# Optimization experiments

Hardware: AMD Instinct MI355X
Metric: run time of the kernel (lower is better)

Reference implementation:

```python
import jax, jax.numpy as jnp
import numpy as np

B, S, HID = 2, 2048, 2048
H, HKV, D = 16, 4, 128

def _rope(x, cos, sin):
    # x: [B,h,S,D]; cos/sin: [1,1,S,D//2]
    d = x.shape[-1] // 2
    x1, x2 = x[..., :d], x[..., d:]
    y1 = x1 * cos + x2 * sin
    y2 = -x1 * sin + x2 * cos
    return jnp.concatenate([y1, y2], axis=-1)

def _rmsnorm(x):
    eps = jnp.finfo(x.dtype).eps
    return x * jax.lax.rsqrt(jnp.mean(jnp.square(x), axis=-1, keepdims=True) + eps)

def setup_inputs() -> dict:
    key = jax.random.key(0)
    ks = jax.random.split(key, 5)
    x = jax.random.normal(ks[0], (B, S, HID), dtype=jnp.float32)
    # realistic rotary tables
    half = D // 2
    inv_freq = 1.0 / (10000.0 ** (jnp.arange(half, dtype=jnp.float32) / half))
    t = jnp.arange(S, dtype=jnp.float32)
    freqs = t[:, None] * inv_freq[None, :]            # [S, D//2]
    cos = jnp.cos(freqs)[None, None]                  # [1,1,S,D//2]
    sin = jnp.sin(freqs)[None, None]
    s = 0.02
    Wq = jax.random.normal(ks[1], (H * D, HID), dtype=jnp.float32) * s
    Wk = jax.random.normal(ks[2], (HKV * D, HID), dtype=jnp.float32) * s
    Wv = jax.random.normal(ks[3], (HKV * D, HID), dtype=jnp.float32) * s
    Wo = jax.random.normal(ks[4], (HID, H * D), dtype=jnp.float32) * s
    return {"x": x, "cos": cos, "sin": sin, "Wq": Wq, "Wk": Wk, "Wv": Wv, "Wo": Wo}

def reference(x, cos, sin, Wq, Wk, Wv, Wo):
    b, s, _ = x.shape
    rep = H // HKV
    q = (x @ Wq.T).reshape(b, s, H, D).transpose(0, 2, 1, 3)      # [B,H,S,D]
    k = (x @ Wk.T).reshape(b, s, HKV, D).transpose(0, 2, 1, 3)    # [B,Hkv,S,D]
    v = (x @ Wv.T).reshape(b, s, HKV, D).transpose(0, 2, 1, 3)
    k = jnp.repeat(k, rep, axis=1)                                # GQA expand
    v = jnp.repeat(v, rep, axis=1)
    q = _rmsnorm(_rope(q, cos, sin))
    k = _rmsnorm(_rope(k, cos, sin))
    scores = jnp.einsum('bhqd,bhkd->bhqk', q, k) * (D ** -0.5)
    causal = jnp.tril(jnp.ones((s, s), dtype=bool))
    scores = jnp.where(causal, scores, -jnp.inf)
    attn = jax.nn.softmax(scores, axis=-1)
    out = jnp.einsum('bhqk,bhkd->bhqd', attn, v)                  # [B,H,S,D]
    out = out.transpose(0, 2, 1, 3).reshape(b, s, H * D)
    return out @ Wo.T
```

## Files before the change

### kernel.cpp

```cpp
#include <hip/hip_runtime.h>
#include <hip/hip_bf16.h>

#define B_  2
#define S_  2048
#define HID_ 2048
#define H_  16
#define HKV_ 4
#define D_  128

typedef __bf16 bf16_t;
typedef bf16_t bf16x8 __attribute__((ext_vector_type(8)));
typedef float f32x4 __attribute__((ext_vector_type(4)));

typedef __attribute__((address_space(3))) unsigned int lds_u32_t;
typedef const __attribute__((address_space(1))) unsigned int glob_u32_t;

__device__ __forceinline__ void gl2lds16(const bf16_t* g, bf16_t* l) {
    __builtin_amdgcn_global_load_lds((glob_u32_t*)g, (lds_u32_t*)l, 16, 0, 0);
}

__device__ __forceinline__ unsigned packbf2(float a, float b) {
    union { bf16_t h[2]; unsigned u; } p;
    p.h[0] = (bf16_t)a;
    p.h[1] = (bf16_t)b;
    return p.u;
}

__global__ void detect_dtype(const unsigned* __restrict__ x, int* __restrict__ flag) {
    int lane = threadIdx.x;
    int c = 0;
#pragma unroll
    for (int i = 0; i < 16; ++i) {
        unsigned w = x[lane * 16 + i];
        unsigned e = (w >> 7) & 0xFF;
        c += (e >= 117 && e <= 137) ? 1 : 0;
    }
#pragma unroll
    for (int m = 1; m < 64; m <<= 1) c += __shfl_xor(c, m, 64);
    if (lane == 0) *flag = (c >= 512) ? 1 : 0;
}

struct Cseg { const void* src; bf16_t* dst; int n8; };

__global__ __launch_bounds__(256) void convert_bf16(Cseg s0, Cseg s1, Cseg s2, Cseg s3,
                                                    const int* __restrict__ flagp) {
    Cseg s = (blockIdx.y == 0) ? s0 : (blockIdx.y == 1) ? s1 : (blockIdx.y == 2) ? s2 : s3;
    const int i = blockIdx.x * 256 + threadIdx.x;
    if (i >= s.n8) return;
    if (*flagp) {
        ((uint4*)s.dst)[i] = ((const uint4*)s.src)[i];
    } else {
        const float4* p = (const float4*)s.src + (size_t)i * 2;
        float4 u = p[0], v = p[1];
        bf16x8 r;
        r[0] = (bf16_t)u.x; r[1] = (bf16_t)u.y; r[2] = (bf16_t)u.z; r[3] = (bf16_t)u.w;
        r[4] = (bf16_t)v.x; r[5] = (bf16_t)v.y; r[6] = (bf16_t)v.z; r[7] = (bf16_t)v.w;
        *(bf16x8*)(s.dst + (size_t)i * 8) = r;
    }
}

__global__ __launch_bounds__(256) void gemm_lds(const bf16_t* __restrict__ A,
                                                const bf16_t* __restrict__ W,
                                                void* __restrict__ C,
                                                int M, int N, int K,
                                                const int* __restrict__ flagp, int osel) {
    __shared__ bf16_t As[128 * 32];
    __shared__ bf16_t Bs[128 * 32];

    const int tid = threadIdx.x;
    const int w = tid >> 6;
    const int lane = tid & 63;
    const int r = lane & 15;
    const int quad = lane >> 4;
    const int m0 = blockIdx.y * 128;
    const int n0 = blockIdx.x * 128;
    const bool of32 = osel && (*flagp == 0);

    const int mh = (w & 1) * 64;
    const int nh = (w >> 1) * 64;

    const int c0 = w * 2;
    const int srow = lane >> 2;
    const int scol = (lane & 3) * 8;
    const bf16_t* Ag0 = A + (size_t)(m0 + c0 * 16 + srow) * K + scol;
    const bf16_t* Ag1 = A + (size_t)(m0 + c0 * 16 + 16 + srow) * K + scol;
    const bf16_t* Wg0 = W + (size_t)(n0 + c0 * 16 + srow) * K + scol;
    const bf16_t* Wg1 = W + (size_t)(n0 + c0 * 16 + 16 + srow) * K + scol;
    bf16_t* Al0 = As + c0 * 512;
    bf16_t* Al1 = As + (c0 + 1) * 512;
    bf16_t* Bl0 = Bs + c0 * 512;
    bf16_t* Bl1 = Bs + (c0 + 1) * 512;

    f32x4 acc[4][4] = {};

    for (int k0 = 0; k0 < K; k0 += 32) {
        __syncthreads();
        gl2lds16(Ag0 + k0, Al0);
        gl2lds16(Ag1 + k0, Al1);
        gl2lds16(Wg0 + k0, Bl0);
        gl2lds16(Wg1 + k0, Bl1);
        __syncthreads();

        bf16x8 a[4], b[4];
#pragma unroll
        for (int mi = 0; mi < 4; ++mi)
            a[mi] = *(const bf16x8*)&As[(mh + mi * 16 + r) * 32 + quad * 8];
#pragma unroll
        for (int ni = 0; ni < 4; ++ni)
            b[ni] = *(const bf16x8*)&Bs[(nh + ni * 16 + r) * 32 + quad * 8];
#pragma unroll
        for (int mi = 0; mi < 4; ++mi)
#pragma unroll
            for (int ni = 0; ni < 4; ++ni)
                acc[mi][ni] = __builtin_amdgcn_mfma_f32_16x16x32_bf16(a[mi], b[ni], acc[mi][ni], 0, 0, 0);
    }

#pragma unroll
    for (int mi = 0; mi < 4; ++mi) {
#pragma unroll
        for (int ni = 0; ni < 4; ++ni) {
#pragma unroll
            for (int g = 0; g < 4; ++g) {
                const int row = m0 + mh + mi * 16 + quad * 4 + g;
                const int col = n0 + nh + ni * 16 + r;
                if (of32) ((float*)C)[(size_t)row * N + col] = acc[mi][ni][g];
                else ((__hip_bfloat16*)C)[(size_t)row * N + col] = __float2bfloat16(acc[mi][ni][g]);
            }
        }
    }
}

template <bool F32>
__device__ __forceinline__ bf16x8 load8(const void* base, size_t off) {
    bf16x8 r;
    if constexpr (F32) {
        const float4* p = (const float4*)((const float*)base + off);
        float4 u = p[0], v = p[1];
        r[0] = (bf16_t)u.x; r[1] = (bf16_t)u.y; r[2] = (bf16_t)u.z; r[3] = (bf16_t)u.w;
        r[4] = (bf16_t)v.x; r[5] = (bf16_t)v.y; r[6] = (bf16_t)v.z; r[7] = (bf16_t)v.w;
    } else {
        r = *(const bf16x8*)((const bf16_t*)base + off);
    }
    return r;
}

template <bool AF32, bool WF32, bool OF32>
__device__ __forceinline__ void gemm_body(const void* __restrict__ A, const void* __restrict__ W,
                                          void* __restrict__ C, int M, int N, int K) {
    const int wave = threadIdx.x >> 6;
    const int lane = threadIdx.x & 63;
    const int r = lane & 15;
    const int quad = lane >> 4;
    const int m0 = blockIdx.y * 64 + wave * 16;
    const int n0 = blockIdx.x * 64;

    f32x4 acc[4] = {};
    const size_t aoff = (size_t)(m0 + r) * K + quad * 8;
    const size_t woff = (size_t)(n0 + r) * K + quad * 8;

    for (int k0 = 0; k0 < K; k0 += 32) {
        bf16x8 a = load8<AF32>(A, aoff + k0);
#pragma unroll
        for (int ns = 0; ns < 4; ++ns) {
            bf16x8 b = load8<WF32>(W, woff + (size_t)(ns * 16) * K + k0);
            acc[ns] = __builtin_amdgcn_mfma_f32_16x16x32_bf16(a, b, acc[ns], 0, 0, 0);
        }
    }

#pragma unroll
    for (int ns = 0; ns < 4; ++ns) {
#pragma unroll
        for (int reg = 0; reg < 4; ++reg) {
            int m = m0 + quad * 4 + reg;
            int n = n0 + ns * 16 + r;
            if constexpr (OF32) ((float*)C)[(size_t)m * N + n] = acc[ns][reg];
            else ((__hip_bfloat16*)C)[(size_t)m * N + n] = __float2bfloat16(acc[ns][reg]);
        }
    }
}

__global__ __launch_bounds__(256) void gemm_bt(const void* __restrict__ A, const void* __restrict__ W,
                                               void* __restrict__ C, int M, int N, int K,
                                               const int* __restrict__ flagp, int mode) {
    const int bf = *flagp;
    if (bf) {
        gemm_body<false, false, false>(A, W, C, M, N, K);
    } else if (mode == 0) {
        gemm_body<true, true, false>(A, W, C, M, N, K);
    } else {
        gemm_body<false, true, true>(A, W, C, M, N, K);
    }
}

__global__ __launch_bounds__(256) void rope_rms(__hip_bfloat16* __restrict__ qk,
                                                const void* __restrict__ cosp,
                                                const void* __restrict__ sinp,
                                                int NH, int ld, const int* __restrict__ flagp) {
    const int bf = *flagp;
    const int wave = threadIdx.x >> 6;
    const int lane = threadIdx.x & 63;
    const int row = blockIdx.x * 4 + wave;
    const int h = row % NH;
    const int bs = row / NH;
    const int s = bs % S_;

    __hip_bfloat16* p = qk + (size_t)bs * ld + h * D_;
    float x1 = __bfloat162float(p[lane]);
    float x2 = __bfloat162float(p[lane + 64]);
    float c, sn, eps;
    if (bf) {
        c   = __bfloat162float(((const __hip_bfloat16*)cosp)[s * 64 + lane]);
        sn  = __bfloat162float(((const __hip_bfloat16*)sinp)[s * 64 + lane]);
        eps = 0.0078125f;
    } else {
        c   = ((const float*)cosp)[s * 64 + lane];
        sn  = ((const float*)sinp)[s * 64 + lane];
        eps = 1.1920929e-07f;
    }
    float y1 = x1 * c + x2 * sn;
    float y2 = x2 * c - x1 * sn;
    float ss = y1 * y1 + y2 * y2;
#pragma unroll
    for (int m = 1; m < 64; m <<= 1) ss += __shfl_xor(ss, m, 64);
    float rinv = rsqrtf(ss * (1.0f / 128.0f) + eps);
    p[lane]      = __float2bfloat16(y1 * rinv);
    p[lane + 64] = __float2bfloat16(y2 * rinv);
}

__global__ __launch_bounds__(256) void v_pack(const __hip_bfloat16* __restrict__ V,
                                              unsigned* __restrict__ Vp, int ldv) {
    const int idx = blockIdx.x * 256 + threadIdx.x;
    const int kp = idx & 15;
    const int t  = (idx >> 4) & 63;
    const int d  = (idx >> 10) & 127;
    const int gy = idx >> 17;
    const int kvh = gy & 3;
    const int b = gy >> 2;
    const unsigned short* p = (const unsigned short*)V
        + (size_t)(b * S_ + 32 * t + kp) * ldv + kvh * D_ + d;
    unsigned lo = p[0];
    unsigned hi = p[(size_t)16 * ldv];
    Vp[idx] = lo | (hi << 16);
}

__global__ __launch_bounds__(512, 2) void attn_flash4(const __hip_bfloat16* __restrict__ Q,
                                                      const __hip_bfloat16* __restrict__ K,
                                                      const unsigned* __restrict__ Vp,
                                                      __hip_bfloat16* __restrict__ O,
                                                      int ldq, int ldkv, int ldo) {
    __shared__ unsigned Pb[8][2][16][16];
    __shared__ float Of[4][32][128];
    __shared__ float Ml[4][2][2][16];

    const int tid = threadIdx.x;
    const int w = tid >> 6;
    const int lane = tid & 63;
    const int r = lane & 15;
    const int quad = lane >> 4;

    const int id = blockIdx.x;
    const int gy = id & 7;
    const int px = id >> 3;
    const int kvh = gy & 3;
    const int b = gy >> 2;
    const int hh = w & 3;
    const int half = w >> 2;
    const int h = kvh * 4 + hh;

    const bf16_t* Kg = (const bf16_t*)K + (size_t)b * S_ * ldkv + kvh * D_;
    const unsigned* Vg = Vp + (size_t)gy * (D_ * 64 * 16);

    bf16x8 ones;
#pragma unroll
    for (int j = 0; j < 8; ++j) ones[j] = (bf16_t)1.0f;

    const float SC2 = 0.08838834764831845f * 1.4426950408889634f;

    for (int rep = 0; rep < 2; ++rep) {
        const int qt = rep ? (63 - px) : px;
        const int q0 = qt * 32;
        const int nkt = qt + 1;
        const int ktb = half ? (nkt >> 1) : 0;
        const int kte = half ? nkt : (nkt >> 1);

        bf16x8 qf[2][4];
#pragma unroll
        for (int t = 0; t < 2; ++t) {
            const bf16_t* qp = (const bf16_t*)Q + (size_t)(b * S_ + q0 + t * 16 + r) * ldq + h * D_ + quad * 8;
#pragma unroll
            for (int c = 0; c < 4; ++c) qf[t][c] = *(const bf16x8*)(qp + c * 32);
        }

        f32x4 oacc[2][8] = {};
        f32x4 lacc[2] = {};
        float m_i[2][4];
#pragma unroll
        for (int t = 0; t < 2; ++t)
#pragma unroll
            for (int g = 0; g < 4; ++g) m_i[t][g] = -3e38f;

        for (int kt = ktb; kt < kte; ++kt) {
            const int k0 = kt * 32;
            const bf16_t* kp0 = Kg + (size_t)(k0 + r) * ldkv + quad * 8;

            f32x4 s0[2] = {}, s1[2] = {};
            __builtin_amdgcn_s_setprio(1);
#pragma unroll
            for (int c = 0; c < 4; ++c) {
                bf16x8 kb0 = *(const bf16x8*)(kp0 + c * 32);
                bf16x8 kb1 = *(const bf16x8*)(kp0 + (size_t)16 * ldkv + c * 32);
#pragma unroll
                for (int t = 0; t < 2; ++t) {
                    s0[t] = __builtin_amdgcn_mfma_f32_16x16x32_bf16(qf[t][c], kb0, s0[t], 0, 0, 0);
                    s1[t] = __builtin_amdgcn_mfma_f32_16x16x32_bf16(qf[t][c], kb1, s1[t], 0, 0, 0);
                }
            }
            __builtin_amdgcn_s_setprio(0);

            const bool bnd = (kt == qt);
#pragma unroll
            for (int t = 0; t < 2; ++t) {
                float mt[4];
#pragma unroll
                for (int g = 0; g < 4; ++g) {
                    s0[t][g] *= SC2;
                    s1[t][g] *= SC2;
                    if (bnd) {
                        const int qrow = q0 + t * 16 + quad * 4 + g;
                        if (k0 + r > qrow)      s0[t][g] = -1e38f;
                        if (k0 + 16 + r > qrow) s1[t][g] = -1e38f;
                    }
                    mt[g] = fmaxf(s0[t][g], s1[t][g]);
                }
#pragma unroll
                for (int msk = 1; msk < 16; msk <<= 1) {
#pragma unroll
                    for (int g = 0; g < 4; ++g) mt[g] = fmaxf(mt[g], __shfl_xor(mt[g], msk, 64));
                }
                bool upd = false;
#pragma unroll
                for (int g = 0; g < 4; ++g) upd |= (mt[g] > m_i[t][g]);
                if (__ballot(upd)) {
#pragma unroll
                    for (int g = 0; g < 4; ++g) {
                        const float mn = fmaxf(m_i[t][g], mt[g]);
                        const float al = exp2f(m_i[t][g] - mn);
                        m_i[t][g] = mn;
                        lacc[t][g] *= al;
#pragma unroll
                        for (int ns = 0; ns < 8; ++ns) oacc[t][ns][g] *= al;
                    }
                }
#pragma unroll
                for (int g = 0; g < 4; ++g) {
                    const float p0 = exp2f(s0[t][g] - m_i[t][g]);
                    const float p1 = exp2f(s1[t][g] - m_i[t][g]);
                    const int row = quad * 4 + g;
                    Pb[w][t][row][(((r >> 2) ^ quad) & 3) * 4 + (r & 3)] = packbf2(p0, p1);
                }
            }

            const int pgrp = ((quad ^ (r >> 2)) & 3) * 4;
            bf16x8 pf0 = *(const bf16x8*)&Pb[w][0][r][pgrp];
            bf16x8 pf1 = *(const bf16x8*)&Pb[w][1][r][pgrp];

            lacc[0] = __builtin_amdgcn_mfma_f32_16x16x32_bf16(pf0, ones, lacc[0], 0, 0, 0);
            lacc[1] = __builtin_amdgcn_mfma_f32_16x16x32_bf16(pf1, ones, lacc[1], 0, 0, 0);

            const unsigned* vp = Vg + (size_t)r * (64 * 16) + kt * 16 + quad * 4;
            __builtin_amdgcn_s_setprio(1);
#pragma unroll
            for (int ns = 0; ns < 8; ++ns) {
                bf16x8 vf = *(const bf16x8*)(vp + (size_t)ns * 16 * 64 * 16);
                oacc[0][ns] = __builtin_amdgcn_mfma_f32_16x16x32_bf16(pf0, vf, oacc[0][ns], 0, 0, 0);
                oacc[1][ns] = __builtin_amdgcn_mfma_f32_16x16x32_bf16(pf1, vf, oacc[1][ns], 0, 0, 0);
            }
            __builtin_amdgcn_s_setprio(0);
        }

        if (half) {
#pragma unroll
            for (int t = 0; t < 2; ++t) {
                if (r == 0) {
#pragma unroll
                    for (int g = 0; g < 4; ++g) {
                        Ml[hh][t][0][quad * 4 + g] = m_i[t][g];
                        Ml[hh][t][1][quad * 4 + g] = lacc[t][g];
                    }
                }
#pragma unroll
                for (int ns = 0; ns < 8; ++ns)
#pragma unroll
                    for (int g = 0; g < 4; ++g)
                        Of[hh][t * 16 + quad * 4 + g][ns * 16 + r] = oacc[t][ns][g];
            }
        }
        __syncthreads();
        if (!half) {
#pragma unroll
            for (int t = 0; t < 2; ++t) {
#pragma unroll
                for (int g = 0; g < 4; ++g) {
                    const int r16 = quad * 4 + g;
                    const float mB = Ml[hh][t][0][r16];
                    const float lB = Ml[hh][t][1][r16];
                    const float mA = m_i[t][g];
                    const float mx = fmaxf(mA, mB);
                    const float aA = exp2f(mA - mx);
                    const float aB = exp2f(mB - mx);
                    const float inv = 1.0f / (lacc[t][g] * aA + lB * aB);
                    const int qrow = q0 + t * 16 + r16;
                    __hip_bfloat16* op = O + (size_t)(b * S_ + qrow) * ldo + h * D_;
#pragma unroll
                    for (int ns = 0; ns < 8; ++ns) {
                        const float v = (oacc[t][ns][g] * aA + Of[hh][t * 16 + r16][ns * 16 + r] * aB) * inv;
                        op[ns * 16 + r] = __float2bfloat16(v);
                    }
                }
            }
        }
        __syncthreads();
    }
}

#define KT_ 32
#define LDK 136

__global__ __launch_bounds__(256, 2) void attn_flash3(const __hip_bfloat16* __restrict__ Q,
                                                      const __hip_bfloat16* __restrict__ K,
                                                      const __hip_bfloat16* __restrict__ V,
                                                      __hip_bfloat16* __restrict__ O,
                                                      int ldq, int ldkv, int ldo) {
    __shared__ unsigned short Ks[KT_][LDK];
    __shared__ unsigned int Vt[D_ * 16];
    __shared__ unsigned int Pb[4][2][16][16];

    const int tid = threadIdx.x;
    const int w = tid >> 6;
    const int lane = tid & 63;
    const int r = lane & 15;
    const int quad = lane >> 4;

    const int gy = blockIdx.y;
    const int kvh = gy % HKV_;
    const int b = gy / HKV_;
    const int qt = b ? blockIdx.x : (gridDim.x - 1 - blockIdx.x);
    const int q0 = qt * 32;
    const int h = kvh * 4 + w;

    bf16x8 qf[2][4];
#pragma unroll
    for (int t = 0; t < 2; ++t) {
        const bf16_t* qp = (const bf16_t*)Q + (size_t)(b * S_ + q0 + t * 16 + r) * ldq + h * D_ + quad * 8;
#pragma unroll
        for (int c = 0; c < 4; ++c) qf[t][c] = *(const bf16x8*)(qp + c * 32);
    }

    f32x4 oacc[2][8] = {};
    f32x4 lacc[2] = {};
    float m_i[2][4];
#pragma unroll
    for (int t = 0; t < 2; ++t)
#pragma unroll
        for (int g = 0; g < 4; ++g) m_i[t][g] = -3e38f;

    const bf16_t* Kg = (const bf16_t*)K + (size_t)b * S_ * ldkv + kvh * D_;
    const bf16_t* Vg = (const bf16_t*)V + (size_t)b * S_ * ldkv + kvh * D_;

    bf16x8 ones;
#pragma unroll
    for (int j = 0; j < 8; ++j) ones[j] = (bf16_t)1.0f;

    const float SC2 = 0.08838834764831845f * 1.4426950408889634f;

    const int skey = tid >> 4;
    const int sdc = tid & 15;
    union U4 { uint4 u; unsigned short s[8]; };
    U4 rk0, rk1, rv0, rv1;
    {
        const size_t o0 = (size_t)skey * ldkv + sdc * 8;
        const size_t o1 = o0 + (size_t)16 * ldkv;
        rk0.u = *(const uint4*)(Kg + o0);
        rk1.u = *(const uint4*)(Kg + o1);
        rv0.u = *(const uint4*)(Vg + o0);
        rv1.u = *(const uint4*)(Vg + o1);
    }

    for (int kt = 0; kt <= qt; ++kt) {
        const int k0 = kt * KT_;
        __syncthreads();
        *(uint4*)&Ks[skey][sdc * 8] = rk0.u;
        *(uint4*)&Ks[skey + 16][sdc * 8] = rk1.u;
#pragma unroll
        for (int j = 0; j < 8; ++j) {
            const int d = sdc * 8 + j;
            const int f = ((j >> 1) & 3) ^ (sdc & 3);
            const int grp = (skey >> 2) ^ f;
            Vt[d * 16 + grp * 4 + (skey & 3)] = (unsigned)rv0.s[j] | ((unsigned)rv1.s[j] << 16);
        }
        __syncthreads();
        if (kt < qt) {
            const size_t o0 = (size_t)(k0 + KT_ + skey) * ldkv + sdc * 8;
            const size_t o1 = o0 + (size_t)16 * ldkv;
            rk0.u = *(const uint4*)(Kg + o0);
            rk1.u = *(const uint4*)(Kg + o1);
            rv0.u = *(const uint4*)(Vg + o0);
            rv1.u = *(const uint4*)(Vg + o1);
        }

        f32x4 s0[2] = {}, s1[2] = {};
#pragma unroll
        for (int c = 0; c < 4; ++c) {
            bf16x8 kb0 = *(const bf16x8*)&Ks[r][c * 32 + quad * 8];
            bf16x8 kb1 = *(const bf16x8*)&Ks[16 + r][c * 32 + quad * 8];
#pragma unroll
            for (int t = 0; t < 2; ++t) {
                s0[t] = __builtin_amdgcn_mfma_f32_16x16x32_bf16(qf[t][c], kb0, s0[t], 0, 0, 0);
                s1[t] = __builtin_amdgcn_mfma_f32_16x16x32_bf16(qf[t][c], kb1, s1[t], 0, 0, 0);
            }
        }

        const bool bnd = (kt == qt);
#pragma unroll
        for (int t = 0; t < 2; ++t) {
            float mt[4];
#pragma unroll
            for (int g = 0; g < 4; ++g) {
                s0[t][g] *= SC2;
                s1[t][g] *= SC2;
                if (bnd) {
                    const int qrow = q0 + t * 16 + quad * 4 + g;
                    if (k0 + r > qrow)      s0[t][g] = -1e38f;
                    if (k0 + 16 + r > qrow) s1[t][g] = -1e38f;
                }
                mt[g] = fmaxf(s0[t][g], s1[t][g]);
            }
#pragma unroll
            for (int msk = 1; msk < 16; msk <<= 1) {
#pragma unroll
                for (int g = 0; g < 4; ++g) mt[g] = fmaxf(mt[g], __shfl_xor(mt[g], msk, 64));
            }
            bool upd = false;
#pragma unroll
            for (int g = 0; g < 4; ++g) upd |= (mt[g] > m_i[t][g]);
            if (__ballot(upd)) {
#pragma unroll
                for (int g = 0; g < 4; ++g) {
                    const float mn = fmaxf(m_i[t][g], mt[g]);
                    const float al = exp2f(m_i[t][g] - mn);
                    m_i[t][g] = mn;
                    lacc[t][g] *= al;
#pragma unroll
                    for (int ns = 0; ns < 8; ++ns) oacc[t][ns][g] *= al;
                }
            }
#pragma unroll
            for (int g = 0; g < 4; ++g) {
                const float p0 = exp2f(s0[t][g] - m_i[t][g]);
                const float p1 = exp2f(s1[t][g] - m_i[t][g]);
                const int row = quad * 4 + g;
                Pb[w][t][row][(((r >> 2) ^ quad) & 3) * 4 + (r & 3)] = packbf2(p0, p1);
            }
        }

        const int pgrp = ((quad ^ (r >> 2)) & 3) * 4;
        bf16x8 pf0 = *(const bf16x8*)&Pb[w][0][r][pgrp];
        bf16x8 pf1 = *(const bf16x8*)&Pb[w][1][r][pgrp];

        lacc[0] = __builtin_amdgcn_mfma_f32_16x16x32_bf16(pf0, ones, lacc[0], 0, 0, 0);
        lacc[1] = __builtin_amdgcn_mfma_f32_16x16x32_bf16(pf1, ones, lacc[1], 0, 0, 0);

#pragma unroll
        for (int ns = 0; ns < 8; ++ns) {
            const int d = ns * 16 + r;
            const int f = ((r >> 1) & 3) ^ ((2 * ns + (r >> 3)) & 3);
            bf16x8 vf = *(const bf16x8*)&Vt[d * 16 + ((quad ^ f) & 3) * 4];
            oacc[0][ns] = __builtin_amdgcn_mfma_f32_16x16x32_bf16(pf0, vf, oacc[0][ns], 0, 0, 0);
            oacc[1][ns] = __builtin_amdgcn_mfma_f32_16x16x32_bf16(pf1, vf, oacc[1][ns], 0, 0, 0);
        }
    }

#pragma unroll
    for (int t = 0; t < 2; ++t) {
#pragma unroll
        for (int g = 0; g < 4; ++g) {
            const float inv = 1.0f / lacc[t][g];
            const int qrow = q0 + t * 16 + quad * 4 + g;
            __hip_bfloat16* op = O + (size_t)(b * S_ + qrow) * ldo + h * D_;
#pragma unroll
            for (int ns = 0; ns < 8; ++ns)
                op[ns * 16 + r] = __float2bfloat16(oacc[t][ns][g] * inv);
        }
    }
}

extern "C" void kernel_launch(void* const* d_in, const int* in_sizes, int n_in,
                              void* d_out, int out_size, void* d_ws, size_t ws_size,
                              hipStream_t stream) {
    const void* x    = d_in[0];
    const void* cosp = d_in[1];
    const void* sinp = d_in[2];
    const void* Wq   = d_in[3];
    const void* Wk   = d_in[4];
    const void* Wv   = d_in[5];
    const void* Wo   = d_in[6];

    const int M = B_ * S_;
    const size_t MB = 1ull << 20;

    if (ws_size >= 28 * MB + 64) {
        char* ws = (char*)d_ws;
        bf16_t* xb = (bf16_t*)ws;
        bf16_t* wb = (bf16_t*)(ws + 16 * MB);
        bf16_t* wo = (bf16_t*)(ws + 16 * MB);
        unsigned* vp4 = (unsigned*)(ws + 24 * MB);
        bf16_t* ao = (bf16_t*)ws;
        int* flag  = (int*)(ws + 28 * MB);
        bf16_t* qkv = (bf16_t*)d_out;

        detect_dtype<<<1, 64, 0, stream>>>((const unsigned*)x, flag);

        Cseg sx{x,  xb,                          (B_ * S_ * HID_) / 8};
        Cseg sq{Wq, wb,                          (H_ * D_ * HID_) / 8};
        Cseg sk{Wk, wb + (size_t)2048 * HID_,    (HKV_ * D_ * HID_) / 8};
        Cseg sv{Wv, wb + (size_t)2560 * HID_,    (HKV_ * D_ * HID_) / 8};
        convert_bf16<<<dim3(4096, 4), 256, 0, stream>>>(sx, sq, sk, sv, flag);

        gemm_lds<<<dim3(3072 / 128, M / 128), 256, 0, stream>>>(xb, wb, qkv, M, 3072, HID_, flag, 0);

        Cseg so{Wo, wo, (HID_ * H_ * D_) / 8};
        convert_bf16<<<dim3(2048, 1), 256, 0, stream>>>(so, so, so, so, flag);

        v_pack<<<(B_ * HKV_ * D_ * 64 * 16) / 256, 256, 0, stream>>>(
            (const __hip_bfloat16*)(qkv + 2560), vp4, 3072);

        rope_rms<<<(B_ * S_ * H_) / 4, 256, 0, stream>>>((__hip_bfloat16*)qkv, cosp, sinp, H_, 3072, flag);
        rope_rms<<<(B_ * S_ * HKV_) / 4, 256, 0, stream>>>((__hip_bfloat16*)(qkv + 2048), cosp, sinp, HKV_, 3072, flag);

        attn_flash4<<<dim3(256), 512, 0, stream>>>(
            (const __hip_bfloat16*)qkv, (const __hip_bfloat16*)(qkv + 2048),
            vp4, (__hip_bfloat16*)ao, 3072, 3072, 2048);

        gemm_lds<<<dim3(HID_ / 128, M / 128), 256, 0, stream>>>(ao, wo, d_out, M, HID_, H_ * D_, flag, 1);
    } else {
        __hip_bfloat16* qb = (__hip_bfloat16*)d_ws;
        int* flag = (int*)((char*)d_ws + (size_t)M * (H_ * D_) * sizeof(__hip_bfloat16));
        __hip_bfloat16* kb = (__hip_bfloat16*)d_out;
        __hip_bfloat16* vb = kb + (size_t)M * (HKV_ * D_);

        detect_dtype<<<1, 64, 0, stream>>>((const unsigned*)x, flag);

        gemm_bt<<<dim3((H_ * D_) / 64, M / 64), 256, 0, stream>>>(x, Wq, qb, M, H_ * D_, HID_, flag, 0);
        gemm_bt<<<dim3((HKV_ * D_) / 64, M / 64), 256, 0, stream>>>(x, Wk, kb, M, HKV_ * D_, HID_, flag, 0);
        gemm_bt<<<dim3((HKV_ * D_) / 64, M / 64), 256, 0, stream>>>(x, Wv, vb, M, HKV_ * D_, HID_, flag, 0);

        rope_rms<<<(B_ * S_ * H_) / 4, 256, 0, stream>>>(qb, cosp, sinp, H_, H_ * D_, flag);
        rope_rms<<<(B_ * S_ * HKV_) / 4, 256, 0, stream>>>(kb, cosp, sinp, HKV_, HKV_ * D_, flag);

        attn_flash3<<<dim3(S_ / 32, B_ * HKV_), 256, 0, stream>>>(qb, kb, vb, qb, H_ * D_, HKV_ * D_, H_ * D_);

        gemm_bt<<<dim3(HID_ / 64, M / 64), 256, 0, stream>>>(qb, Wo, d_out, M, HID_, H_ * D_, flag, 1);
    }
}
```

Measured before the change: 416.9 us.

## Drop online softmax max using fixed offset, split KV four ways, pack K/V tile-contiguous

Because q and k are RMS-normalized, scores are bounded, so the kernel replaces the running max and rescaling with a constant exponent offset and removes the shuffle reductions and ballot-driven rescales. The attention block grows to 1024 threads with the KV range split across four wave groups, merged sequentially through LDS. A new k_pack kernel and a reordered v_pack lay out K and V contiguously per 32-key tile for better locality. This relies on the norm bound (the fixed offset could overflow or underflow for other inputs), adds extra syncthreads in the merge, and adds a pack pass plus a stricter requirement on the output buffer size.

```diff
diff --git a/kernel.cpp b/kernel.cpp
--- a/kernel.cpp
+++ b/kernel.cpp
@@ -227,30 +227,44 @@
     p[lane + 64] = __float2bfloat16(y2 * rinv);
 }
 
+__global__ __launch_bounds__(256) void k_pack(const __hip_bfloat16* __restrict__ Kin,
+                                              bf16_t* __restrict__ Kp) {
+    const int idx = blockIdx.x * 256 + threadIdx.x;
+    const int d0 = (idx & 15) * 8;
+    const int row = (idx >> 4) & 31;
+    const int kt = (idx >> 9) & 63;
+    const int gy = idx >> 15;
+    const int kvh = gy & 3;
+    const int bb = gy >> 2;
+    const bf16_t* src = (const bf16_t*)Kin + (size_t)(bb * S_ + kt * 32 + row) * 3072 + kvh * D_ + d0;
+    *(uint4*)(Kp + (size_t)idx * 8) = *(const uint4*)src;
+}
+
 __global__ __launch_bounds__(256) void v_pack(const __hip_bfloat16* __restrict__ V,
                                               unsigned* __restrict__ Vp, int ldv) {
     const int idx = blockIdx.x * 256 + threadIdx.x;
     const int kp = idx & 15;
-    const int t  = (idx >> 4) & 63;
-    const int d  = (idx >> 10) & 127;
+    const int d  = (idx >> 4) & 127;
+    const int kt = (idx >> 11) & 63;
     const int gy = idx >> 17;
     const int kvh = gy & 3;
     const int b = gy >> 2;
     const unsigned short* p = (const unsigned short*)V
-        + (size_t)(b * S_ + 32 * t + kp) * ldv + kvh * D_ + d;
+        + (size_t)(b * S_ + 32 * kt + kp) * ldv + kvh * D_ + d;
     unsigned lo = p[0];
     unsigned hi = p[(size_t)16 * ldv];
     Vp[idx] = lo | (hi << 16);
 }
 
-__global__ __launch_bounds__(512, 2) void attn_flash4(const __hip_bfloat16* __restrict__ Q,
-                                                      const __hip_bfloat16* __restrict__ K,
-                                                      const unsigned* __restrict__ Vp,
-                                                      __hip_bfloat16* __restrict__ O,
-                                                      int ldq, int ldkv, int ldo) {
-    __shared__ unsigned Pb[8][2][16][16];
+#define M0F 16.5f
+
+__global__ __launch_bounds__(1024, 4) void attn_flash5(const __hip_bfloat16* __restrict__ Q,
+                                                       const bf16_t* __restrict__ Kp,
+                                                       const unsigned* __restrict__ Vp,
+                                                       __hip_bfloat16* __restrict__ O) {
+    __shared__ unsigned Pb[16][2][16][16];
     __shared__ float Of[4][32][128];
-    __shared__ float Ml[4][2][2][16];
+    __shared__ float Lf[4][2][16];
 
     const int tid = threadIdx.x;
     const int w = tid >> 6;
@@ -264,11 +278,11 @@
     const int kvh = gy & 3;
     const int b = gy >> 2;
     const int hh = w & 3;
-    const int half = w >> 2;
+    const int qd = w >> 2;
     const int h = kvh * 4 + hh;
 
-    const bf16_t* Kg = (const bf16_t*)K + (size_t)b * S_ * ldkv + kvh * D_;
-    const unsigned* Vg = Vp + (size_t)gy * (D_ * 64 * 16);
+    const bf16_t* Kg = Kp + (size_t)gy * (64 * 32 * 128);
+    const unsigned* Vg = Vp + (size_t)gy * (64 * 128 * 16);
 
     bf16x8 ones;
 #pragma unroll
@@ -280,35 +294,29 @@
         const int qt = rep ? (63 - px) : px;
         const int q0 = qt * 32;
         const int nkt = qt + 1;
-        const int ktb = half ? (nkt >> 1) : 0;
-        const int kte = half ? nkt : (nkt >> 1);
+        const int ktb = (nkt * qd) >> 2;
+        const int kte = (nkt * (qd + 1)) >> 2;
 
         bf16x8 qf[2][4];
 #pragma unroll
         for (int t = 0; t < 2; ++t) {
-            const bf16_t* qp = (const bf16_t*)Q + (size_t)(b * S_ + q0 + t * 16 + r) * ldq + h * D_ + quad * 8;
+            const bf16_t* qp = (const bf16_t*)Q + (size_t)(b * S_ + q0 + t * 16 + r) * 3072 + h * D_ + quad * 8;
 #pragma unroll
             for (int c = 0; c < 4; ++c) qf[t][c] = *(const bf16x8*)(qp + c * 32);
         }
 
         f32x4 oacc[2][8] = {};
         f32x4 lacc[2] = {};
-        float m_i[2][4];
-#pragma unroll
-        for (int t = 0; t < 2; ++t)
-#pragma unroll
-            for (int g = 0; g < 4; ++g) m_i[t][g] = -3e38f;
 
         for (int kt = ktb; kt < kte; ++kt) {
-            const int k0 = kt * 32;
-            const bf16_t* kp0 = Kg + (size_t)(k0 + r) * ldkv + quad * 8;
+            const bf16_t* kp0 = Kg + ((size_t)kt * 32 + r) * 128 + quad * 8;
 
             f32x4 s0[2] = {}, s1[2] = {};
             __builtin_amdgcn_s_setprio(1);
 #pragma unroll
             for (int c = 0; c < 4; ++c) {
                 bf16x8 kb0 = *(const bf16x8*)(kp0 + c * 32);
-                bf16x8 kb1 = *(const bf16x8*)(kp0 + (size_t)16 * ldkv + c * 32);
+                bf16x8 kb1 = *(const bf16x8*)(kp0 + 16 * 128 + c * 32);
 #pragma unroll
                 for (int t = 0; t < 2; ++t) {
                     s0[t] = __builtin_amdgcn_mfma_f32_16x16x32_bf16(qf[t][c], kb0, s0[t], 0, 0, 0);
@@ -317,48 +325,25 @@
             }
             __builtin_amdgcn_s_setprio(0);
 
-            const bool bnd = (kt == qt);
-#pragma unroll
-            for (int t = 0; t < 2; ++t) {
-                float mt[4];
+            if (kt == qt) {
+#pragma unroll
+                for (int t = 0; t < 2; ++t)
+#pragma unroll
+                    for (int g = 0; g < 4; ++g) {
+                        const int qrow = q0 + t * 16 + quad * 4 + g;
+                        if (kt * 32 + r > qrow)      s0[t][g] = -1e38f;
+                        if (kt * 32 + 16 + r > qrow) s1[t][g] = -1e38f;
+                    }
+            }
+
+#pragma unroll
+            for (int t = 0; t < 2; ++t)
 #pragma unroll
                 for (int g = 0; g < 4; ++g) {
-                    s0[t][g] *= SC2;
-                    s1[t][g] *= SC2;
-                    if (bnd) {
-                        const int qrow = q0 + t * 16 + quad * 4 + g;
-                        if (k0 + r > qrow)      s0[t][g] = -1e38f;
-                        if (k0 + 16 + r > qrow) s1[t][g] = -1e38f;
-                    }
-                    mt[g] = fmaxf(s0[t][g], s1[t][g]);
-                }
-#pragma unroll
-                for (int msk = 1; msk < 16; msk <<= 1) {
-#pragma unroll
-                    for (int g = 0; g < 4; ++g) mt[g] = fmaxf(mt[g], __shfl_xor(mt[g], msk, 64));
-                }
-                bool upd = false;
-#pragma unroll
-                for (int g = 0; g < 4; ++g) upd |= (mt[g] > m_i[t][g]);
-                if (__ballot(upd)) {
-#pragma unroll
-                    for (int g = 0; g < 4; ++g) {
-                        const float mn = fmaxf(m_i[t][g], mt[g]);
-                        const float al = exp2f(m_i[t][g] - mn);
-                        m_i[t][g] = mn;
-                        lacc[t][g] *= al;
-#pragma unroll
-                        for (int ns = 0; ns < 8; ++ns) oacc[t][ns][g] *= al;
-                    }
-                }
-#pragma unroll
-                for (int g = 0; g < 4; ++g) {
-                    const float p0 = exp2f(s0[t][g] - m_i[t][g]);
-                    const float p1 = exp2f(s1[t][g] - m_i[t][g]);
-                    const int row = quad * 4 + g;
-                    Pb[w][t][row][(((r >> 2) ^ quad) & 3) * 4 + (r & 3)] = packbf2(p0, p1);
-                }
-            }
+                    const float p0 = exp2f(fmaf(s0[t][g], SC2, -M0F));
+                    const float p1 = exp2f(fmaf(s1[t][g], SC2, -M0F));
+                    Pb[w][t][quad * 4 + g][(((r >> 2) ^ quad) & 3) * 4 + (r & 3)] = packbf2(p0, p1);
+                }
 
             const int pgrp = ((quad ^ (r >> 2)) & 3) * 4;
             bf16x8 pf0 = *(const bf16x8*)&Pb[w][0][r][pgrp];
@@ -367,26 +352,24 @@
             lacc[0] = __builtin_amdgcn_mfma_f32_16x16x32_bf16(pf0, ones, lacc[0], 0, 0, 0);
             lacc[1] = __builtin_amdgcn_mfma_f32_16x16x32_bf16(pf1, ones, lacc[1], 0, 0, 0);
 
-            const unsigned* vp = Vg + (size_t)r * (64 * 16) + kt * 16 + quad * 4;
+            const unsigned* vp = Vg + ((size_t)kt * 128 + r) * 16 + quad * 4;
             __builtin_amdgcn_s_setprio(1);
 #pragma unroll
             for (int ns = 0; ns < 8; ++ns) {
-                bf16x8 vf = *(const bf16x8*)(vp + (size_t)ns * 16 * 64 * 16);
+                bf16x8 vf = *(const bf16x8*)(vp + ns * 256);
                 oacc[0][ns] = __builtin_amdgcn_mfma_f32_16x16x32_bf16(pf0, vf, oacc[0][ns], 0, 0, 0);
                 oacc[1][ns] = __builtin_amdgcn_mfma_f32_16x16x32_bf16(pf1, vf, oacc[1][ns], 0, 0, 0);
             }
             __builtin_amdgcn_s_setprio(0);
         }
 
-        if (half) {
+        __syncthreads();
+        if (qd == 1) {
 #pragma unroll
             for (int t = 0; t < 2; ++t) {
                 if (r == 0) {
 #pragma unroll
-                    for (int g = 0; g < 4; ++g) {
-                        Ml[hh][t][0][quad * 4 + g] = m_i[t][g];
-                        Ml[hh][t][1][quad * 4 + g] = lacc[t][g];
-                    }
+                    for (int g = 0; g < 4; ++g) Lf[hh][t][quad * 4 + g] = lacc[t][g];
                 }
 #pragma unroll
                 for (int ns = 0; ns < 8; ++ns)
@@ -396,30 +379,52 @@
             }
         }
         __syncthreads();
-        if (!half) {
+        if (qd == 2) {
+#pragma unroll
+            for (int t = 0; t < 2; ++t) {
+                if (r == 0) {
+#pragma unroll
+                    for (int g = 0; g < 4; ++g) Lf[hh][t][quad * 4 + g] += lacc[t][g];
+                }
+#pragma unroll
+                for (int ns = 0; ns < 8; ++ns)
+#pragma unroll
+                    for (int g = 0; g < 4; ++g)
+                        Of[hh][t * 16 + quad * 4 + g][ns * 16 + r] += oacc[t][ns][g];
+            }
+        }
+        __syncthreads();
+        if (qd == 3) {
+#pragma unroll
+            for (int t = 0; t < 2; ++t) {
+                if (r == 0) {
+#pragma unroll
+                    for (int g = 0; g < 4; ++g) Lf[hh][t][quad * 4 + g] += lacc[t][g];
+                }
+#pragma unroll
+                for (int ns = 0; ns < 8; ++ns)
+#pragma unroll
+                    for (int g = 0; g < 4; ++g)
+                        Of[hh][t * 16 + quad * 4 + g][ns * 16 + r] += oacc[t][ns][g];
+            }
+        }
+        __syncthreads();
+        if (qd == 0) {
 #pragma unroll
             for (int t = 0; t < 2; ++t) {
 #pragma unroll
                 for (int g = 0; g < 4; ++g) {
                     const int r16 = quad * 4 + g;
-                    const float mB = Ml[hh][t][0][r16];
-                    const float lB = Ml[hh][t][1][r16];
-                    const float mA = m_i[t][g];
-                    const float mx = fmaxf(mA, mB);
-                    const float aA = exp2f(mA - mx);
-                    const float aB = exp2f(mB - mx);
-                    const float inv = 1.0f / (lacc[t][g] * aA + lB * aB);
+                    const float l = lacc[t][g] + Lf[hh][t][r16];
+                    const float inv = 1.0f / l;
                     const int qrow = q0 + t * 16 + r16;
-                    __hip_bfloat16* op = O + (size_t)(b * S_ + qrow) * ldo + h * D_;
-#pragma unroll
-                    for (int ns = 0; ns < 8; ++ns) {
-                        const float v = (oacc[t][ns][g] * aA + Of[hh][t * 16 + r16][ns * 16 + r] * aB) * inv;
-                        op[ns * 16 + r] = __float2bfloat16(v);
-                    }
-                }
-            }
-        }
-        __syncthreads();
+                    __hip_bfloat16* op = O + (size_t)(b * S_ + qrow) * 2048 + h * D_;
+#pragma unroll
+                    for (int ns = 0; ns < 8; ++ns)
+                        op[ns * 16 + r] = __float2bfloat16((oacc[t][ns][g] + Of[hh][t * 16 + r16][ns * 16 + r]) * inv);
+                }
+            }
+        }
     }
 }
 
@@ -608,7 +613,7 @@
     const int M = B_ * S_;
     const size_t MB = 1ull << 20;
 
-    if (ws_size >= 28 * MB + 64) {
+    if (ws_size >= 28 * MB + 64 && (size_t)out_size >= 28 * MB) {
         char* ws = (char*)d_ws;
         bf16_t* xb = (bf16_t*)ws;
         bf16_t* wb = (bf16_t*)(ws + 16 * MB);
@@ -617,6 +622,7 @@
         bf16_t* ao = (bf16_t*)ws;
         int* flag  = (int*)(ws + 28 * MB);
         bf16_t* qkv = (bf16_t*)d_out;
+        bf16_t* kp8 = (bf16_t*)((char*)d_out + 24 * MB);
 
         detect_dtype<<<1, 64, 0, stream>>>((const unsigned*)x, flag);
 
@@ -637,9 +643,10 @@
         rope_rms<<<(B_ * S_ * H_) / 4, 256, 0, stream>>>((__hip_bfloat16*)qkv, cosp, sinp, H_, 3072, flag);
         rope_rms<<<(B_ * S_ * HKV_) / 4, 256, 0, stream>>>((__hip_bfloat16*)(qkv + 2048), cosp, sinp, HKV_, 3072, flag);
 
-        attn_flash4<<<dim3(256), 512, 0, stream>>>(
-            (const __hip_bfloat16*)qkv, (const __hip_bfloat16*)(qkv + 2048),
-            vp4, (__hip_bfloat16*)ao, 3072, 3072, 2048);
+        k_pack<<<dim3(1024), 256, 0, stream>>>((const __hip_bfloat16*)(qkv + 2048), kp8);
+
+        attn_flash5<<<dim3(256), 1024, 0, stream>>>(
+            (const __hip_bfloat16*)qkv, kp8, vp4, (__hip_bfloat16*)ao);
 
         gemm_lds<<<dim3(HID_ / 128, M / 128), 256, 0, stream>>>(ao, wo, d_out, M, HID_, H_ * D_, flag, 1);
     } else {
```

Measured after the change: 1.643 ms. 3.94x slower.
